# Performance work log

Measured on AMD Instinct MI355X. Metric: run time of the kernel, lower is better.

## Reference

```python
import jax, jax.numpy as jnp
import numpy as np

jax.config.update("jax_enable_x64", True)  # hash uses int64 multiply-xor like torch .long()

NUM_LEVELS = 16
LEVEL_DIM = 2
PER_LEVEL_SCALE = 2
BASE_RES = 16
LOG2_HASHMAP = 19
PS1 = 19349663  # second spatial hash prime (ps[0] == 1)
N_POINTS = 524288


def _isprime(n):
    for p in range(2, int(n ** 0.5) + 1):
        if n % p == 0:
            return False
    return True


N_ENTRIES = 2 ** LOG2_HASHMAP
while not _isprime(N_ENTRIES):
    N_ENTRIES += 1  # -> 524309

SCALES = []
OFFSETS = [0]
START_HASH = NUM_LEVELS  # module uses -1 sentinel; NUM_LEVELS == 'no hashing yet'
for i in range(NUM_LEVELS):
    res = int(BASE_RES * PER_LEVEL_SCALE ** i)
    SCALES.append(res)
    n = (res + 1) ** 2
    if n > N_ENTRIES:
        if START_HASH == NUM_LEVELS:
            START_HASH = i
        n = N_ENTRIES
    OFFSETS.append(OFFSETS[-1] + n)
TABLE_SIZE = OFFSETS[-1]  # 5594552

CORNERS = jnp.array([[0.0, 0.0], [0.0, 1.0], [1.0, 0.0], [1.0, 1.0]], dtype=jnp.float32)  # [4,2]
SCALES_F = jnp.array(SCALES, dtype=jnp.float32)          # [L]
SCALES_I = jnp.array(SCALES, dtype=jnp.int64)            # [L]
LEVEL_OFF = jnp.array(OFFSETS[:-1], dtype=jnp.int64)     # [L] base offset per level


def setup_inputs() -> dict:
    key = jax.random.key(0)
    k1, k2 = jax.random.split(key)
    x = jax.random.uniform(k1, (N_POINTS, 2), dtype=jnp.float32)  # coords in [0,1)
    data = (jax.random.uniform(k2, (TABLE_SIZE, LEVEL_DIM), dtype=jnp.float32) * 2.0 - 1.0) * 1e-4
    return {"x": x, "data": data}


def reference(x, data):
    L, F = NUM_LEVELS, LEVEL_DIM
    float_x = x[None] * SCALES_F[:, None, None]                                  # [L,N,2]
    int_x = (float_x[:, :, None, :] + CORNERS[None, None]).astype(jnp.int64)     # [L,N,4,2]
    offset_x = float_x - int_x[:, :, 0].astype(float_x.dtype)                    # [L,N,2] frac part
    ix0, ix1 = int_x[..., 0], int_x[..., 1]
    # dense-grid index for low levels, spatial hash for high levels
    grid_ind = ix0 * (SCALES_I + 1)[:, None, None] + ix1                         # [L,N,4]
    hash_ind = (ix0 ^ (ix1 * PS1)) % N_ENTRIES                                   # [L,N,4]
    is_grid = (jnp.arange(L) < START_HASH)[:, None, None]
    ind = jnp.where(is_grid, grid_ind, hash_ind) + LEVEL_OFF[:, None, None]      # [L,N,4]
    val = data[ind]                                                              # [L,N,4,F]
    # bilinear corner weights: clamp(1 - c + (2c-1)*frac) per axis, product over xy
    w = jnp.clip(1.0 - CORNERS[None, None] + (2.0 * CORNERS[None, None] - 1.0) * offset_x[:, :, None], 0.0, 1.0)
    w = w[..., 0] * w[..., 1]                                                    # [L,N,4]
    out = jnp.einsum('lnc,lncf->lnf', w, val)                                    # [L,N,F]
    return out.transpose(1, 0, 2).reshape(-1, L * F)                             # [N, L*F]
```

## Files before the change

kernel.cpp:

```cpp
#include <hip/hip_runtime.h>


static constexpr int  kPoints    = 524288;
static constexpr int  kLevels    = 16;
static constexpr int  kStartHash = 6;
static constexpr long long kPs1     = 19349663LL;
static constexpr long long kEntries = 524309LL;

__constant__ long long c_level_off[kLevels] = {
    0LL, 289LL, 1378LL, 5603LL, 22244LL, 88293LL, 351462LL,
    875771LL, 1400080LL, 1924389LL, 2448698LL, 2973007LL,
    3497316LL, 4021625LL, 4545934LL, 5070243LL
};

__device__ __forceinline__ float2 interp_level(
    const float2 p, const float2* __restrict__ tbl, const int l)
{
    const int   scale_i = 16 << l;
    const float scale_f = (float)scale_i;

    const float fx = p.x * scale_f;
    const float fy = p.y * scale_f;

    const long long ix0 = (long long)fx;
    const long long iy0 = (long long)fy;
    const long long ix1 = (long long)(fx + 1.0f);
    const long long iy1 = (long long)(fy + 1.0f);

    const float ox = fx - (float)ix0;
    const float oy = fy - (float)iy0;

    const float wx1 = fminf(fmaxf(ox, 0.0f), 1.0f);
    const float wx0 = fminf(fmaxf(1.0f - ox, 0.0f), 1.0f);
    const float wy1 = fminf(fmaxf(oy, 0.0f), 1.0f);
    const float wy0 = fminf(fmaxf(1.0f - oy, 0.0f), 1.0f);

    long long i00, i01, i10, i11;
    if (l < kStartHash) {
        const long long stride = (long long)(scale_i + 1);
        i00 = ix0 * stride + iy0;
        i01 = ix0 * stride + iy1;
        i10 = ix1 * stride + iy0;
        i11 = ix1 * stride + iy1;
    } else {
        const long long hy0 = iy0 * kPs1;
        const long long hy1 = iy1 * kPs1;
        i00 = (ix0 ^ hy0) % kEntries;
        i01 = (ix0 ^ hy1) % kEntries;
        i10 = (ix1 ^ hy0) % kEntries;
        i11 = (ix1 ^ hy1) % kEntries;
    }

    const long long base = c_level_off[l];
    const float2 v00 = tbl[base + i00];
    const float2 v01 = tbl[base + i01];
    const float2 v10 = tbl[base + i10];
    const float2 v11 = tbl[base + i11];

    const float w00 = wx0 * wy0;
    const float w01 = wx0 * wy1;
    const float w10 = wx1 * wy0;
    const float w11 = wx1 * wy1;

    return make_float2(
        w00 * v00.x + w01 * v01.x + w10 * v10.x + w11 * v11.x,
        w00 * v00.y + w01 * v01.y + w10 * v10.y + w11 * v11.y);
}

__global__ __launch_bounds__(256) void level_pass(
    const float2* __restrict__ x,
    const float2* __restrict__ tbl,
    float2* __restrict__ ws)
{
    const int b    = blockIdx.x;
    const int xcd  = b & 7;
    const int slot = b >> 3;

    int level, pblk;
    if (slot < 2048) {
        level = 6 + xcd;
        pblk  = slot;
    } else if (slot < 2304) {
        level = 14;
        pblk  = xcd * 256 + (slot - 2048);
    } else if (slot < 2560) {
        level = 15;
        pblk  = xcd * 256 + (slot - 2304);
    } else {
        const int d = xcd * 1536 + (slot - 2560);
        level = d >> 11;
        pblk  = d & 2047;
    }

    const int n = (pblk << 8) | threadIdx.x;
    const float2 p = x[n];
    ws[(size_t)level * kPoints + n] = interp_level(p, tbl, level);
}

static constexpr int kTStride = 257;

__global__ __launch_bounds__(256) void transpose_out(
    const float2* __restrict__ ws,
    float4* __restrict__ out)
{
    __shared__ float2 lds[kLevels * kTStride];

    const int t  = threadIdx.x;
    const int n0 = blockIdx.x * 256;

#pragma unroll
    for (int l = 0; l < kLevels; ++l)
        lds[l * kTStride + t] = ws[(size_t)l * kPoints + n0 + t];

    __syncthreads();

    float4* o = out + (size_t)n0 * 8;
#pragma unroll
    for (int k = 0; k < 8; ++k) {
        const int f  = k * 256 + t;
        const int nl = f >> 3;
        const int i  = t & 7;
        const float2 a = lds[(2 * i)     * kTStride + nl];
        const float2 b = lds[(2 * i + 1) * kTStride + nl];
        o[f] = make_float4(a.x, a.y, b.x, b.y);
    }
}

__global__ __launch_bounds__(256) void hashgrid_fwd(
    const float2* __restrict__ x,
    const float2* __restrict__ tbl,
    float4* __restrict__ out)
{
    const int n = blockIdx.x * blockDim.x + threadIdx.x;
    if (n >= kPoints) return;
    const float2 p = x[n];
    float acc[2 * kLevels];
#pragma unroll
    for (int l = 0; l < kLevels; ++l) {
        const float2 r = interp_level(p, tbl, l);
        acc[2 * l + 0] = r.x;
        acc[2 * l + 1] = r.y;
    }
    float4* o = out + (size_t)n * 8;
#pragma unroll
    for (int i = 0; i < 8; ++i)
        o[i] = make_float4(acc[4 * i + 0], acc[4 * i + 1],
                           acc[4 * i + 2], acc[4 * i + 3]);
}

extern "C" void kernel_launch(void* const* d_in, const int* in_sizes, int n_in,
                              void* d_out, int out_size, void* d_ws, size_t ws_size,
                              hipStream_t stream) {
    const float2* x   = (const float2*)d_in[0];
    const float2* tbl = (const float2*)d_in[1];

    const size_t ws_needed = (size_t)kLevels * kPoints * sizeof(float2);
    if (ws_size >= ws_needed) {
        float2* ws = (float2*)d_ws;
        level_pass<<<kLevels * (kPoints / 256), 256, 0, stream>>>(x, tbl, ws);
        transpose_out<<<kPoints / 256, 256, 0, stream>>>(ws, (float4*)d_out);
    } else {
        hashgrid_fwd<<<kPoints / 256, 256, 0, stream>>>(x, tbl, (float4*)d_out);
    }
}
```

Before: 227.8 us.

## Replace 64-bit hash modulo with 32-bit split arithmetic and tile workspace per block

The spatial hash modulo is rewritten to use 32-bit operations. The 64-bit product is split into high and low words, and the high word is reduced using the precomputed constant 2^32 mod P. This avoids costly 64-bit integer division on the GPU. Indices and offsets also move to 32-bit. The workspace layout changes from level-major to point-block-major tiles, so the transpose kernel reads one contiguous 32KB tile per block. Correctness depends on the modular decomposition matching the reference for nonnegative coordinates.

```diff
diff --git a/kernel.cpp b/kernel.cpp
--- a/kernel.cpp
+++ b/kernel.cpp
@@ -4,13 +4,14 @@
 static constexpr int  kPoints    = 524288;
 static constexpr int  kLevels    = 16;
 static constexpr int  kStartHash = 6;
-static constexpr long long kPs1     = 19349663LL;
-static constexpr long long kEntries = 524309LL;
+static constexpr unsigned kPs1     = 19349663u;
+static constexpr unsigned kEntries = 524309u;
+static constexpr unsigned kR32     = 352277u;
 
-__constant__ long long c_level_off[kLevels] = {
-    0LL, 289LL, 1378LL, 5603LL, 22244LL, 88293LL, 351462LL,
-    875771LL, 1400080LL, 1924389LL, 2448698LL, 2973007LL,
-    3497316LL, 4021625LL, 4545934LL, 5070243LL
+__constant__ unsigned c_level_off[kLevels] = {
+    0u, 289u, 1378u, 5603u, 22244u, 88293u, 351462u,
+    875771u, 1400080u, 1924389u, 2448698u, 2973007u,
+    3497316u, 4021625u, 4545934u, 5070243u
 };
 
 __device__ __forceinline__ float2 interp_level(
@@ -22,10 +23,10 @@
     const float fx = p.x * scale_f;
     const float fy = p.y * scale_f;
 
-    const long long ix0 = (long long)fx;
-    const long long iy0 = (long long)fy;
-    const long long ix1 = (long long)(fx + 1.0f);
-    const long long iy1 = (long long)(fy + 1.0f);
+    const unsigned ix0 = (unsigned)(int)fx;
+    const unsigned iy0 = (unsigned)(int)fy;
+    const unsigned ix1 = (unsigned)(int)(fx + 1.0f);
+    const unsigned iy1 = (unsigned)(int)(fy + 1.0f);
 
     const float ox = fx - (float)ix0;
     const float oy = fy - (float)iy0;
@@ -35,23 +36,27 @@
     const float wy1 = fminf(fmaxf(oy, 0.0f), 1.0f);
     const float wy0 = fminf(fmaxf(1.0f - oy, 0.0f), 1.0f);
 
-    long long i00, i01, i10, i11;
+    unsigned i00, i01, i10, i11;
     if (l < kStartHash) {
-        const long long stride = (long long)(scale_i + 1);
+        const unsigned stride = (unsigned)(scale_i + 1);
         i00 = ix0 * stride + iy0;
         i01 = ix0 * stride + iy1;
         i10 = ix1 * stride + iy0;
         i11 = ix1 * stride + iy1;
     } else {
-        const long long hy0 = iy0 * kPs1;
-        const long long hy1 = iy1 * kPs1;
-        i00 = (ix0 ^ hy0) % kEntries;
-        i01 = (ix0 ^ hy1) % kEntries;
-        i10 = (ix1 ^ hy0) % kEntries;
-        i11 = (ix1 ^ hy1) % kEntries;
+        const unsigned long long hy0 = (unsigned long long)iy0 * kPs1;
+        const unsigned long long hy1 = (unsigned long long)iy1 * kPs1;
+        const unsigned lo0 = (unsigned)hy0, hi0 = (unsigned)(hy0 >> 32);
+        const unsigned lo1 = (unsigned)hy1, hi1 = (unsigned)(hy1 >> 32);
+        const unsigned a0 = (hi0 * kR32) % kEntries;
+        const unsigned a1 = (hi1 * kR32) % kEntries;
+        i00 = a0 + ((lo0 ^ ix0) % kEntries); if (i00 >= kEntries) i00 -= kEntries;
+        i01 = a1 + ((lo1 ^ ix0) % kEntries); if (i01 >= kEntries) i01 -= kEntries;
+        i10 = a0 + ((lo0 ^ ix1) % kEntries); if (i10 >= kEntries) i10 -= kEntries;
+        i11 = a1 + ((lo1 ^ ix1) % kEntries); if (i11 >= kEntries) i11 -= kEntries;
     }
 
-    const long long base = c_level_off[l];
+    const unsigned base = c_level_off[l];
     const float2 v00 = tbl[base + i00];
     const float2 v01 = tbl[base + i01];
     const float2 v10 = tbl[base + i10];
@@ -94,7 +99,8 @@
 
     const int n = (pblk << 8) | threadIdx.x;
     const float2 p = x[n];
-    ws[(size_t)level * kPoints + n] = interp_level(p, tbl, level);
+    ws[((size_t)pblk << 12) + (level << 8) + threadIdx.x] =
+        interp_level(p, tbl, level);
 }
 
 static constexpr int kTStride = 257;
@@ -105,16 +111,16 @@
 {
     __shared__ float2 lds[kLevels * kTStride];
 
-    const int t  = threadIdx.x;
-    const int n0 = blockIdx.x * 256;
+    const int t = threadIdx.x;
+    const float2* __restrict__ tile = ws + ((size_t)blockIdx.x << 12);
 
 #pragma unroll
     for (int l = 0; l < kLevels; ++l)
-        lds[l * kTStride + t] = ws[(size_t)l * kPoints + n0 + t];
+        lds[l * kTStride + t] = tile[(l << 8) + t];
 
     __syncthreads();
 
-    float4* o = out + (size_t)n0 * 8;
+    float4* o = out + ((size_t)blockIdx.x << 11);
 #pragma unroll
     for (int k = 0; k < 8; ++k) {
         const int f  = k * 256 + t;
```

Result: faster. 222.6 us (-2.3%).
